# Kernel optimization log

Hardware: AMD Instinct MI355X
Metric: run time of the kernel (lower is better)

Reference implementation:

```python
import jax, jax.numpy as jnp
import numpy as np

B, F, D = 1024, 16, 64
P = F * (F - 1) // 2  # 120 field pairs


def setup_inputs() -> dict:
    key = jax.random.key(0)
    k1, k2, k3 = jax.random.split(key, 3)
    x = jax.random.normal(k1, (B, F, D), dtype=jnp.float32)
    # torch Linear weight layout: [out_features, in_features] = [D, D*D], one per pair
    W = jax.random.normal(k2, (P, D, D * D), dtype=jnp.float32) * (1.0 / np.sqrt(D * D))
    b = jax.random.normal(k3, (P, D), dtype=jnp.float32) * 0.01
    return {"x": x, "W": W, "b": b}


def reference(x, W, b):
    # x: [B, F, D]; W: [P, D, D*D]; b: [P, D]
    Bs, Fs, Ds = x.shape
    Ps = W.shape[0]
    ii, jj = np.triu_indices(Fs, k=1)  # pair order matches nested (i, j>i) loop
    xi = x[:, ii, :]  # [B, P, D] -> left vector of outer product
    xj = x[:, jj, :]  # [B, P, D] -> right vector
    # Flattened outer tmp[b, a*D + c] = xi[b,p,a] * xj[b,p,c];
    # Linear: out = tmp @ W^T + b. Reshape W to [P, D_out, a, c] and fuse,
    # never materializing the [B, P, D*D] outer-product tensor.
    W3 = W.reshape(Ps, Ds, Ds, Ds)
    out = jnp.einsum('bpa,bpc,pkac->bpk', xi, xj, W3) + b[None, :, :]
    return out  # [B, P, D]
```

## Files before the change

### kernel.cpp

```cpp
#include <hip/hip_runtime.h>
#include <stdint.h>
#include <stddef.h>

constexpr int NB = 1024;
constexpr int NF = 16;
constexpr int ND = 64;
constexpr int NP = 120;
constexpr int KD = ND * ND;
constexpr int OUT_STRIDE = NP * ND;

constexpr int BM = 128;

using floatx4 = __attribute__((ext_vector_type(4))) float;
using half8   = __attribute__((ext_vector_type(8))) _Float16;
using half2v  = __attribute__((ext_vector_type(2))) _Float16;
using fp16x2  = __attribute__((ext_vector_type(2))) __fp16;
using uint4v  = __attribute__((ext_vector_type(4))) uint32_t;

constexpr int XT_STRIDE = BM;
constexpr int BT_STRIDE = 72;
constexpr int BT_BUF    = ND * BT_STRIDE;

__device__ __forceinline__ half2v pkh2(float f0, float f1) {
    fp16x2 h = __builtin_amdgcn_cvt_pkrtz(f0, f1);
    return __builtin_bit_cast(half2v, h);
}
__device__ __forceinline__ uint32_t pk16(float f0, float f1) {
    fp16x2 h = __builtin_amdgcn_cvt_pkrtz(f0, f1);
    return __builtin_bit_cast(uint32_t, h);
}
__device__ __forceinline__ uint16_t f16bits(float f) {
    return __builtin_bit_cast(uint16_t, (_Float16)f);
}

__global__ __launch_bounds__(256, 4)
void outer_kernel(const float* __restrict__ x, const float* __restrict__ W,
                  const float* __restrict__ bias, float* __restrict__ out)
{
    __shared__ uint16_t lds_xit[ND * XT_STRIDE];
    __shared__ uint16_t lds_bt[2 * BT_BUF];

    const int p  = blockIdx.x;
    const int b0 = blockIdx.y * BM;

    int icol = 0, rem = p;
    while (rem >= NF - 1 - icol) { rem -= NF - 1 - icol; ++icol; }
    const int jcol = icol + 1 + rem;

    const int t    = threadIdx.x;
    const int wave = t >> 6;
    const int lane = t & 63;
    const int r    = lane & 15;
    const int quad = lane >> 4;

    {
        const int mrow  = t >> 1;
        const int chalf = (t & 1) * 32;
        const float* src = x + (size_t)(b0 + mrow) * (NF * ND) + icol * ND + chalf;
        #pragma unroll
        for (int c = 0; c < 32; c += 4) {
            floatx4 v = *(const floatx4*)(src + c);
            lds_xit[(chalf + c + 0) * XT_STRIDE + mrow] = f16bits(v.x);
            lds_xit[(chalf + c + 1) * XT_STRIDE + mrow] = f16bits(v.y);
            lds_xit[(chalf + c + 2) * XT_STRIDE + mrow] = f16bits(v.z);
            lds_xit[(chalf + c + 3) * XT_STRIDE + mrow] = f16bits(v.w);
        }
    }

    half2v xjh[2][8];
    #pragma unroll
    for (int ms = 0; ms < 2; ++ms) {
        const float* srow = x + (size_t)(b0 + wave*32 + ms*16 + r) * (NF * ND)
                              + jcol * ND + quad * 8;
        #pragma unroll
        for (int ks = 0; ks < 2; ++ks) {
            floatx4 v0 = *(const floatx4*)(srow + ks * 32);
            floatx4 v1 = *(const floatx4*)(srow + ks * 32 + 4);
            xjh[ms][ks*4 + 0] = pkh2(v0.x, v0.y);
            xjh[ms][ks*4 + 1] = pkh2(v0.z, v0.w);
            xjh[ms][ks*4 + 2] = pkh2(v1.x, v1.y);
            xjh[ms][ks*4 + 3] = pkh2(v1.z, v1.w);
        }
    }

    const int n_st = t >> 2;
    const int c_st = (t & 3) * 16;
    const float* wsrc = W + ((size_t)p * ND + n_st) * KD + c_st;
    uint16_t* bdst0 = &lds_bt[n_st * BT_STRIDE + c_st];

    floatx4 wreg[4];

    #pragma unroll
    for (int q = 0; q < 4; ++q) wreg[q] = *(const floatx4*)(wsrc + q * 4);
    {
        uint4v q0 = (uint4v){ pk16(wreg[0].x, wreg[0].y), pk16(wreg[0].z, wreg[0].w),
                              pk16(wreg[1].x, wreg[1].y), pk16(wreg[1].z, wreg[1].w) };
        uint4v q1 = (uint4v){ pk16(wreg[2].x, wreg[2].y), pk16(wreg[2].z, wreg[2].w),
                              pk16(wreg[3].x, wreg[3].y), pk16(wreg[3].z, wreg[3].w) };
        *(uint4v*)(bdst0)     = q0;
        *(uint4v*)(bdst0 + 8) = q1;
    }
    #pragma unroll
    for (int q = 0; q < 4; ++q) wreg[q] = *(const floatx4*)(wsrc + ND + q * 4);
    __syncthreads();

    floatx4 acc[2][4] = {};

    #pragma unroll 1
    for (int a = 0; a < ND; ++a) {
        const int cur = a & 1;
        const uint16_t* rbuf = lds_bt + cur * BT_BUF;

        uint32_t xiu[2];
        #pragma unroll
        for (int ms = 0; ms < 2; ++ms)
            xiu[ms] = lds_xit[a * XT_STRIDE + wave*32 + ms*16 + r];

        half8 bfr[4][2];
        #pragma unroll
        for (int ns = 0; ns < 4; ++ns) {
            const int brow = (ns*16 + r) * BT_STRIDE + quad * 8;
            bfr[ns][0] = *(const half8*)&rbuf[brow];
            bfr[ns][1] = *(const half8*)&rbuf[brow + 32];
        }

        half8 pa0[2], pa1[2];
        #pragma unroll
        for (int ms = 0; ms < 2; ++ms) {
            half2v xs = __builtin_bit_cast(half2v,
                __builtin_amdgcn_perm(xiu[ms], xiu[ms], 0x01000100u));
            union { half8 h8; half2v h2[4]; } u0, u1;
            #pragma unroll
            for (int q2 = 0; q2 < 4; ++q2) {
                u0.h2[q2] = xs * xjh[ms][q2];
                u1.h2[q2] = xs * xjh[ms][4 + q2];
            }
            pa0[ms] = u0.h8;
            pa1[ms] = u1.h8;
        }

        #pragma unroll
        for (int ns = 0; ns < 4; ++ns) {
            #pragma unroll
            for (int ms = 0; ms < 2; ++ms) {
                acc[ms][ns] = __builtin_amdgcn_mfma_f32_16x16x32_f16(
                    pa0[ms], bfr[ns][0], acc[ms][ns], 0, 0, 0);
                acc[ms][ns] = __builtin_amdgcn_mfma_f32_16x16x32_f16(
                    pa1[ms], bfr[ns][1], acc[ms][ns], 0, 0, 0);
            }
        }

        if (a + 1 < ND) {
            uint16_t* bd = bdst0 + (cur ^ 1) * BT_BUF;
            uint4v q0 = (uint4v){ pk16(wreg[0].x, wreg[0].y), pk16(wreg[0].z, wreg[0].w),
                                  pk16(wreg[1].x, wreg[1].y), pk16(wreg[1].z, wreg[1].w) };
            uint4v q1 = (uint4v){ pk16(wreg[2].x, wreg[2].y), pk16(wreg[2].z, wreg[2].w),
                                  pk16(wreg[3].x, wreg[3].y), pk16(wreg[3].z, wreg[3].w) };
            *(uint4v*)(bd)     = q0;
            *(uint4v*)(bd + 8) = q1;
        }
        if (a + 2 < ND) {
            const float* wn = wsrc + (size_t)(a + 2) * ND;
            #pragma unroll
            for (int q = 0; q < 4; ++q) wreg[q] = *(const floatx4*)(wn + q * 4);
        }

        __syncthreads();
    }

    #pragma unroll
    for (int ns = 0; ns < 4; ++ns) {
        const float bb = bias[p * ND + ns*16 + r];
        #pragma unroll
        for (int ms = 0; ms < 2; ++ms) {
            #pragma unroll
            for (int reg = 0; reg < 4; ++reg) {
                const int row = b0 + wave*32 + ms*16 + quad*4 + reg;
                out[(size_t)row * OUT_STRIDE + p * ND + ns*16 + r]
                    = acc[ms][ns][reg] + bb;
            }
        }
    }
}

extern "C" void kernel_launch(void* const* d_in, const int* in_sizes, int n_in,
                              void* d_out, int out_size, void* d_ws, size_t ws_size,
                              hipStream_t stream) {
    const float* x    = (const float*)d_in[0];
    const float* W    = (const float*)d_in[1];
    const float* bias = (const float*)d_in[2];
    float* out = (float*)d_out;

    dim3 grid(NP, NB / BM);
    outer_kernel<<<grid, 256, 0, stream>>>(x, W, bias, out);
}
```

Measured before the change: 255.9 us.

## Double batch tile to 256 rows with 512 threads and XOR-swizzled W tile in LDS

```diff
diff --git a/kernel.cpp b/kernel.cpp
--- a/kernel.cpp
+++ b/kernel.cpp
@@ -9,7 +9,7 @@
 constexpr int KD = ND * ND;
 constexpr int OUT_STRIDE = NP * ND;
 
-constexpr int BM = 128;
+constexpr int BM = 256;
 
 using floatx4 = __attribute__((ext_vector_type(4))) float;
 using half8   = __attribute__((ext_vector_type(8))) _Float16;
@@ -18,7 +18,7 @@
 using uint4v  = __attribute__((ext_vector_type(4))) uint32_t;
 
 constexpr int XT_STRIDE = BM;
-constexpr int BT_STRIDE = 72;
+constexpr int BT_STRIDE = ND;
 constexpr int BT_BUF    = ND * BT_STRIDE;
 
 __device__ __forceinline__ half2v pkh2(float f0, float f1) {
@@ -33,7 +33,7 @@
     return __builtin_bit_cast(uint16_t, (_Float16)f);
 }
 
-__global__ __launch_bounds__(256, 4)
+__global__ __launch_bounds__(512, 4)
 void outer_kernel(const float* __restrict__ x, const float* __restrict__ W,
                   const float* __restrict__ bias, float* __restrict__ out)
 {
@@ -83,28 +83,27 @@
         }
     }
 
-    const int n_st = t >> 2;
-    const int c_st = (t & 3) * 16;
-    const float* wsrc = W + ((size_t)p * ND + n_st) * KD + c_st;
-    uint16_t* bdst0 = &lds_bt[n_st * BT_STRIDE + c_st];
+    const int n_st = t >> 3;
+    const int cg   = t & 7;
+    const float* wsrc = W + ((size_t)p * ND + n_st) * KD + cg * 8;
+    uint16_t* bdst0 = &lds_bt[n_st * BT_STRIDE + ((cg ^ (n_st & 7)) * 8)];
 
-    floatx4 wreg[4];
+    floatx4 wreg[2];
 
-    #pragma unroll
-    for (int q = 0; q < 4; ++q) wreg[q] = *(const floatx4*)(wsrc + q * 4);
+    wreg[0] = *(const floatx4*)(wsrc);
+    wreg[1] = *(const floatx4*)(wsrc + 4);
     {
         uint4v q0 = (uint4v){ pk16(wreg[0].x, wreg[0].y), pk16(wreg[0].z, wreg[0].w),
                               pk16(wreg[1].x, wreg[1].y), pk16(wreg[1].z, wreg[1].w) };
-        uint4v q1 = (uint4v){ pk16(wreg[2].x, wreg[2].y), pk16(wreg[2].z, wreg[2].w),
-                              pk16(wreg[3].x, wreg[3].y), pk16(wreg[3].z, wreg[3].w) };
-        *(uint4v*)(bdst0)     = q0;
-        *(uint4v*)(bdst0 + 8) = q1;
+        *(uint4v*)(bdst0) = q0;
     }
-    #pragma unroll
-    for (int q = 0; q < 4; ++q) wreg[q] = *(const floatx4*)(wsrc + ND + q * 4);
+    wreg[0] = *(const floatx4*)(wsrc + ND);
+    wreg[1] = *(const floatx4*)(wsrc + ND + 4);
     __syncthreads();
 
     floatx4 acc[2][4] = {};
+
+    const int xg0 = (quad ^ (r & 7)) * 8;
 
     #pragma unroll 1
     for (int a = 0; a < ND; ++a) {
@@ -119,9 +118,9 @@
         half8 bfr[4][2];
         #pragma unroll
         for (int ns = 0; ns < 4; ++ns) {
-            const int brow = (ns*16 + r) * BT_STRIDE + quad * 8;
-            bfr[ns][0] = *(const half8*)&rbuf[brow];
-            bfr[ns][1] = *(const half8*)&rbuf[brow + 32];
+            const int rowb = (ns*16 + r) * BT_STRIDE;
+            bfr[ns][0] = *(const half8*)&rbuf[rowb + xg0];
+            bfr[ns][1] = *(const half8*)&rbuf[rowb + (xg0 ^ 32)];
         }
 
         half8 pa0[2], pa1[2];
@@ -154,15 +153,12 @@
             uint16_t* bd = bdst0 + (cur ^ 1) * BT_BUF;
             uint4v q0 = (uint4v){ pk16(wreg[0].x, wreg[0].y), pk16(wreg[0].z, wreg[0].w),
                                   pk16(wreg[1].x, wreg[1].y), pk16(wreg[1].z, wreg[1].w) };
-            uint4v q1 = (uint4v){ pk16(wreg[2].x, wreg[2].y), pk16(wreg[2].z, wreg[2].w),
-                                  pk16(wreg[3].x, wreg[3].y), pk16(wreg[3].z, wreg[3].w) };
-            *(uint4v*)(bd)     = q0;
-            *(uint4v*)(bd + 8) = q1;
+            *(uint4v*)(bd) = q0;
         }
         if (a + 2 < ND) {
             const float* wn = wsrc + (size_t)(a + 2) * ND;
-            #pragma unroll
-            for (int q = 0; q < 4; ++q) wreg[q] = *(const floatx4*)(wn + q * 4);
+            wreg[0] = *(const floatx4*)(wn);
+            wreg[1] = *(const floatx4*)(wn + 4);
         }
 
         __syncthreads();
@@ -192,5 +188,5 @@
     float* out = (float*)d_out;
 
     dim3 grid(NP, NB / BM);
-    outer_kernel<<<grid, 256, 0, stream>>>(x, W, bias, out);
+    outer_kernel<<<grid, 512, 0, stream>>>(x, W, bias, out);
 }
```

New measurement: 219.0 us. 14.4% less time.
